# Optimization experiments

Hardware: AMD Instinct MI355X
Metric: run time of the kernel (lower is better)

## Reference

```python
import jax, jax.numpy as jnp
import numpy as np

N_NODES = 50000
N_REL = 8
N_EDGES = 400000  # per relation
D_IN = 256
D_OUT = 256


def setup_inputs() -> dict:
    key = jax.random.key(0)
    k1, k2, k3, k4, k5 = jax.random.split(key, 5)
    gain = np.sqrt(2.0)  # relu gain used by xavier init in the module
    x = jax.random.normal(k1, (N_NODES, D_IN), dtype=jnp.float32)
    weight = jax.random.normal(k2, (N_REL, D_IN, D_OUT), dtype=jnp.float32) * (gain / np.sqrt(D_IN + D_OUT))
    h_bias = jnp.zeros((D_OUT,), dtype=jnp.float32)
    loop_weight = jax.random.normal(k3, (D_IN, D_OUT), dtype=jnp.float32) * (gain / np.sqrt(D_IN + D_OUT))
    src_idx = jax.random.randint(k4, (N_REL, N_EDGES), 0, N_NODES, dtype=jnp.int32)
    dst_idx = jax.random.randint(k5, (N_REL, N_EDGES), 0, N_NODES, dtype=jnp.int32)
    return {"x": x, "weight": weight, "h_bias": h_bias, "loop_weight": loop_weight,
            "src_idx": src_idx, "dst_idx": dst_idx}


def reference(x, weight, h_bias, loop_weight, src_idx, dst_idx):
    # x: [N, D_in]; weight: [R, D_in, D_out]; src/dst_idx: [R, E]
    n = x.shape[0]
    out = jnp.zeros((n, weight.shape[-1]), dtype=x.dtype)
    # Loop over the small fixed set of relations (structurally distinct weights).
    for r in range(weight.shape[0]):
        h = x @ weight[r]                                   # [N, D_out] transform-first (in<=out path of GraphConv)
        msg = h[src_idx[r]]                                 # [E, D_out] gather
        agg = jax.ops.segment_sum(msg, dst_idx[r], num_segments=n)  # [N, D_out] scatter-add
        deg = jax.ops.segment_sum(jnp.ones((dst_idx.shape[1],), dtype=x.dtype),
                                  dst_idx[r], num_segments=n)
        out = out + agg / jnp.clip(deg, 1.0)[:, None]       # norm='right': divide by in-degree (clamped at 1)
    out = out + x @ loop_weight + h_bias                    # self-loop + bias
    return jax.nn.relu(out)                                  # activation; dropout(p=0) is identity
```

## Files before the change

### kernel.cpp

```cpp
#include <hip/hip_runtime.h>
#include <hip/hip_bf16.h>

#define NN 50000
#define NPAD 50048
#define NR 8
#define NE 400000
#define CAP 32
#define CHUNK 2048
#define CPB 196
#define NRANGE 6250
#define XBLK 12500
#define TBLK 144

typedef __attribute__((ext_vector_type(8))) short short8v;
typedef __attribute__((ext_vector_type(4))) float f32x4;
typedef __attribute__((ext_vector_type(2))) unsigned int uint2v;

static __device__ __forceinline__ ushort f2b(float f) {
  union { float f; unsigned u; } v; v.f = f;
  unsigned u = v.u;
  unsigned r = (u + 0x7fffu + ((u >> 16) & 1u)) >> 16;
  return (ushort)r;
}
static __device__ __forceinline__ float b2f(ushort u) {
  union { unsigned u; float f; } v; v.u = ((unsigned)u) << 16;
  return v.f;
}


__global__ __launch_bounds__(256) void k_prep(const float* __restrict__ x,
                                              const float* __restrict__ w,
                                              const float* __restrict__ lw,
                                              ushort* __restrict__ xb,
                                              ushort* __restrict__ wb,
                                              const int* __restrict__ src,
                                              const int* __restrict__ dst,
                                              int* __restrict__ cnt,
                                              ushort* __restrict__ csrp) {
  __shared__ ushort tile[64][66];
  int b = blockIdx.x;
  if (b < XBLK) {
    int i = b * 256 + threadIdx.x;
    float4 v = ((const float4*)x)[i];
    ushort4 o;
    o.x = f2b(v.x); o.y = f2b(v.y); o.z = f2b(v.z); o.w = f2b(v.w);
    ((ushort4*)xb)[i] = o;
    return;
  }
  if (b < XBLK + TBLK) {
    int tb = b - XBLK;
    int s = tb >> 4, t16 = tb & 15;
    int kt = (t16 >> 2) * 64, nt2 = (t16 & 3) * 64;
    const float* srcw = (s < 8) ? (w + (size_t)s * 65536) : lw;
    int t = threadIdx.x;
    #pragma unroll
    for (int i = 0; i < 16; ++i) {
      int flat = i * 256 + t;
      int kk = flat >> 6, nn = flat & 63;
      tile[kk][nn] = f2b(srcw[(size_t)(kt + kk) * 256 + nt2 + nn]);
    }
    __syncthreads();
    #pragma unroll
    for (int i = 0; i < 16; ++i) {
      int flat = i * 256 + t;
      int nn2 = flat >> 6, kk2 = flat & 63;
      wb[(size_t)s * 65536 + (size_t)(nt2 + nn2) * 256 + kt + kk2] = tile[kk2][nn2];
    }
    return;
  }
  int xcd = b & 7;
  int rc = (b - XBLK - TBLK) >> 3;
  int r = rc / CPB;
  int c = rc - r * CPB;
  int nlo = xcd * NRANGE, nhi = nlo + NRANGE;
  const int* dr = dst + (size_t)r * NE;
  const int* sr = src + (size_t)r * NE;
  int e0 = c * CHUNK + threadIdx.x * 4;
  #pragma unroll
  for (int u = 0; u < CHUNK / 1024; ++u) {
    int e = e0 + u * 1024;
    if (e + 3 < NE) {
      int4 d4 = *(const int4*)(dr + e);
      int4 s4 = *(const int4*)(sr + e);
      #pragma unroll
      for (int k = 0; k < 4; ++k) {
        int d = (k == 0) ? d4.x : (k == 1) ? d4.y : (k == 2) ? d4.z : d4.w;
        int s = (k == 0) ? s4.x : (k == 1) ? s4.y : (k == 2) ? s4.z : s4.w;
        if (d >= nlo && d < nhi) {
          int slot = atomicAdd(&cnt[r * NN + d], 1);
          if (slot < CAP)
            csrp[((size_t)r * NN + d) * CAP + slot] = (ushort)s;
        }
      }
    } else {
      for (int k = 0; k < 4; ++k) {
        int e2 = e + k;
        if (e2 < NE) {
          int d = dr[e2];
          if (d >= nlo && d < nhi) {
            int slot = atomicAdd(&cnt[r * NN + d], 1);
            if (slot < CAP)
              csrp[((size_t)r * NN + d) * CAP + slot] = (ushort)sr[e2];
          }
        }
      }
    }
  }
}


__global__ __launch_bounds__(256) void k_agg(const ushort* __restrict__ xb,
                                             const ushort* __restrict__ csrp,
                                             const int* __restrict__ cnt,
                                             ushort* __restrict__ xa,
                                             long strideR, int r0) {
  int wid = threadIdx.x >> 6, lane = threadIdx.x & 63;
  int n = blockIdx.x * 4 + wid;
  int r = r0 + blockIdx.y;
  if (n >= NN) return;
  int dg = cnt[r * NN + n];
  int m = min(dg, CAP);
  const ushort* lst = csrp + ((size_t)r * NN + n) * CAP;
  float a0 = 0.f, a1 = 0.f, a2 = 0.f, a3 = 0.f;
  int j = 0;
  for (; j + 3 < m; j += 4) {
    int s0 = lst[j], s1 = lst[j + 1], s2 = lst[j + 2], s3 = lst[j + 3];
    ushort4 v0 = *(const ushort4*)(xb + (size_t)s0 * 256 + lane * 4);
    ushort4 v1 = *(const ushort4*)(xb + (size_t)s1 * 256 + lane * 4);
    ushort4 v2 = *(const ushort4*)(xb + (size_t)s2 * 256 + lane * 4);
    ushort4 v3 = *(const ushort4*)(xb + (size_t)s3 * 256 + lane * 4);
    a0 += (b2f(v0.x) + b2f(v1.x)) + (b2f(v2.x) + b2f(v3.x));
    a1 += (b2f(v0.y) + b2f(v1.y)) + (b2f(v2.y) + b2f(v3.y));
    a2 += (b2f(v0.z) + b2f(v1.z)) + (b2f(v2.z) + b2f(v3.z));
    a3 += (b2f(v0.w) + b2f(v1.w)) + (b2f(v2.w) + b2f(v3.w));
  }
  for (; j < m; ++j) {
    ushort4 v0 = *(const ushort4*)(xb + (size_t)lst[j] * 256 + lane * 4);
    a0 += b2f(v0.x); a1 += b2f(v0.y); a2 += b2f(v0.z); a3 += b2f(v0.w);
  }
  float inv = 1.f / (float)max(dg, 1);
  unsigned w0 = ((unsigned)f2b(a0 * inv)) | (((unsigned)f2b(a1 * inv)) << 16);
  unsigned w1 = ((unsigned)f2b(a2 * inv)) | (((unsigned)f2b(a3 * inv)) << 16);
  uint2v o; o[0] = w0; o[1] = w1;
  __builtin_nontemporal_store(o, (uint2v*)(xa + (size_t)(r - r0) * strideR +
                                           (size_t)n * 256 + lane * 4));
}


#define BK 64

__global__ __launch_bounds__(512, 4) void k_gemm(
    const ushort* __restrict__ xa, long strideR, int nseg,
    const ushort* __restrict__ xb8, const ushort* __restrict__ wb, int wseg0,
    const float* __restrict__ bias, float* __restrict__ out, int first, int final_) {
  __shared__ ushort As[2][128 * BK];
  __shared__ ushort Bs[256 * BK];
  int t = threadIdx.x;
  int lane = t & 63, wid = t >> 6;
  int wm = wid >> 2, wn = wid & 3;
  int i0 = blockIdx.x * 128;
  const int NT = nseg * 4;

  f32x4 acc[4][4];
  #pragma unroll
  for (int a = 0; a < 4; ++a)
    #pragma unroll
    for (int b = 0; b < 4; ++b) acc[a][b] = (f32x4){0.f, 0.f, 0.f, 0.f};

#define STAGE_A(stp, buf) do {                                                  \
    int s_ = (stp) >> 2; int kt_ = ((stp) & 3) * 64;                            \
    const ushort* A_ = (wseg0 + s_ < 8) ? (xa + (size_t)s_ * strideR) : xb8;    \
    _Pragma("unroll")                                                           \
    for (int it = 0; it < 2; ++it) {                                            \
      int c = it * 512 + t; int row = c >> 3, sg = c & 7;                       \
      int sgg = sg ^ (row & 7);                                                 \
      const ushort* ga = A_ + (size_t)(i0 + row) * 256 + kt_ + sgg * 8;         \
      __builtin_amdgcn_global_load_lds(                                         \
          (const __attribute__((address_space(1))) unsigned int*)ga,            \
          (__attribute__((address_space(3))) unsigned int*)(As[buf] + c * 8),   \
          16, 0, 0);                                                            \
    } } while (0)

#define STAGE_B(stp) do {                                                       \
    int s_ = (stp) >> 2; int kt_ = ((stp) & 3) * 64;                            \
    const ushort* W_ = wb + (size_t)(wseg0 + s_) * 65536;                       \
    _Pragma("unroll")                                                           \
    for (int it = 0; it < 4; ++it) {                                            \
      int c = it * 512 + t; int row = c >> 3, sg = c & 7;                       \
      int sgg = sg ^ (row & 7);                                                 \
      const ushort* gb = W_ + (size_t)row * 256 + kt_ + sgg * 8;                \
      __builtin_amdgcn_global_load_lds(                                         \
          (const __attribute__((address_space(1))) unsigned int*)gb,            \
          (__attribute__((address_space(3))) unsigned int*)(Bs + c * 8),        \
          16, 0, 0);                                                            \
    } } while (0)

  STAGE_A(0, 0);
  int cur = 0;
  #pragma unroll 1
  for (int st = 0; st < NT; ++st) {
    __builtin_amdgcn_s_barrier();
    STAGE_B(st);
    if (st + 1 < NT) {
      STAGE_A(st + 1, cur ^ 1);
      asm volatile("s_waitcnt vmcnt(2)" ::: "memory");
    } else {
      asm volatile("s_waitcnt vmcnt(0)" ::: "memory");
    }
    __builtin_amdgcn_sched_barrier(0);
    __builtin_amdgcn_s_barrier();
    __builtin_amdgcn_sched_barrier(0);
    const ushort* Ac = As[cur];
    #pragma unroll
    for (int kk = 0; kk < 2; ++kk) {
      int ko = kk * 32 + (lane >> 4) * 8;
      int kb = ko * 2;
      short8v a_frag[4], b_frag[4];
      #pragma unroll
      for (int mi = 0; mi < 4; ++mi) {
        int row = wm * 64 + mi * 16 + (lane & 15);
        int ba = row * 128 + (kb ^ ((row & 7) << 4));
        a_frag[mi] = *(const short8v*)((const char*)Ac + ba);
      }
      #pragma unroll
      for (int ni = 0; ni < 4; ++ni) {
        int row = wn * 64 + ni * 16 + (lane & 15);
        int ba = row * 128 + (kb ^ ((row & 7) << 4));
        b_frag[ni] = *(const short8v*)((const char*)Bs + ba);
      }
      #pragma unroll
      for (int mi = 0; mi < 4; ++mi)
        #pragma unroll
        for (int ni = 0; ni < 4; ++ni)
          acc[mi][ni] = __builtin_amdgcn_mfma_f32_16x16x32_bf16(
              a_frag[mi], b_frag[ni], acc[mi][ni], 0, 0, 0);
    }
    cur ^= 1;
  }
#undef STAGE_A
#undef STAGE_B

  #pragma unroll
  for (int mi = 0; mi < 4; ++mi) {
    int rbase = i0 + wm * 64 + mi * 16 + ((lane >> 4) << 2);
    #pragma unroll
    for (int ni = 0; ni < 4; ++ni) {
      int col = wn * 64 + ni * 16 + (lane & 15);
      float bv = final_ ? bias[col] : 0.f;
      #pragma unroll
      for (int rg = 0; rg < 4; ++rg) {
        int gm = rbase + rg;
        if (gm < NN) {
          size_t o = (size_t)gm * 256 + col;
          float v = acc[mi][ni][rg];
          if (!first) v += out[o];
          if (final_) v = fmaxf(v + bv, 0.f);
          out[o] = v;
        }
      }
    }
  }
}


extern "C" void kernel_launch(void* const* d_in, const int* in_sizes, int n_in,
                              void* d_out, int out_size, void* d_ws, size_t ws_size,
                              hipStream_t stream) {
  const float* x = (const float*)d_in[0];
  const float* w = (const float*)d_in[1];
  const float* bias = (const float*)d_in[2];
  const float* lw = (const float*)d_in[3];
  const int* src = (const int*)d_in[4];
  const int* dst = (const int*)d_in[5];
  float* out = (float*)d_out;

  char* ws = (char*)d_ws;
  size_t off = 0;
  auto carve = [&](size_t bytes) {
    size_t o = off;
    off = (off + bytes + 255) & ~(size_t)255;
    return o;
  };
  int* cnt = (int*)(ws + carve((size_t)NR * NN * 4));
  ushort* csrp = (ushort*)(ws + carve((size_t)NR * NN * CAP * 2));
  ushort* wb = (ushort*)(ws + carve((size_t)9 * 65536 * 2));
  ushort* xb = (ushort*)(ws + carve((size_t)NPAD * 256 * 2));
  size_t base_bytes = off;
  ushort* xa = (ushort*)(ws + off);
  const size_t segb = (size_t)NPAD * 256 * 2;
  long strideR = (long)NPAD * 256;

  (void)hipMemsetAsync(cnt, 0, (size_t)NR * NN * 4, stream);
  k_prep<<<XBLK + TBLK + 8 * CPB * NR, 256, 0, stream>>>(x, w, lw, xb, wb,
                                                         src, dst, cnt, csrp);

  dim3 gemm_grid(NPAD / 128);
  if (ws_size >= base_bytes + 8 * segb) {
    k_agg<<<dim3((NN + 3) / 4, 8), 256, 0, stream>>>(xb, csrp, cnt, xa, strideR, 0);
    k_gemm<<<gemm_grid, 512, 0, stream>>>(xa, strideR, 9, xb, wb, 0, bias, out, 1, 1);
  } else if (ws_size >= base_bytes + 4 * segb) {
    k_agg<<<dim3((NN + 3) / 4, 4), 256, 0, stream>>>(xb, csrp, cnt, xa, strideR, 0);
    k_gemm<<<gemm_grid, 512, 0, stream>>>(xa, strideR, 4, xb, wb, 0, bias, out, 1, 0);
    k_agg<<<dim3((NN + 3) / 4, 4), 256, 0, stream>>>(xb, csrp, cnt, xa, strideR, 4);
    k_gemm<<<gemm_grid, 512, 0, stream>>>(xa, strideR, 5, xb, wb, 4, bias, out, 0, 1);
  } else {
    for (int r = 0; r < 8; ++r) {
      k_agg<<<dim3((NN + 3) / 4, 1), 256, 0, stream>>>(xb, csrp, cnt, xa, strideR, r);
      k_gemm<<<gemm_grid, 512, 0, stream>>>(xa, strideR, 1, xb, wb, r, bias, out,
                                            (r == 0) ? 1 : 0, 0);
    }
    k_gemm<<<gemm_grid, 512, 0, stream>>>(xa, strideR, 1, xb, wb, 8, bias, out, 0, 1);
  }
  (void)in_sizes; (void)n_in; (void)out_size;
}
```

Baseline: 453.6 us.

## Use column-chunked bf16 layout so gather aggregation stays cache-resident per chunk

Stores bf16 x and the aggregated features as 8 column chunks of 32 features ([8][NPAD][32]) instead of row-major. The aggregation kernel processes one chunk per grid z-slice, using 8 threads per destination node, so each pass gathers from a much smaller working set that can stay in cache. The GEMM A-tile loads are re-addressed for the chunked layout. The cost is smaller, less contiguous gather segments and 8x more aggregation blocks that each re-read CSR lists and counts.

```diff
diff --git a/kernel.cpp b/kernel.cpp
--- a/kernel.cpp
+++ b/kernel.cpp
@@ -28,10 +28,11 @@
 }
 
 
+
 __global__ __launch_bounds__(256) void k_prep(const float* __restrict__ x,
                                               const float* __restrict__ w,
                                               const float* __restrict__ lw,
-                                              ushort* __restrict__ xb,
+                                              ushort* __restrict__ xbc,
                                               ushort* __restrict__ wb,
                                               const int* __restrict__ src,
                                               const int* __restrict__ dst,
@@ -41,10 +42,11 @@
   int b = blockIdx.x;
   if (b < XBLK) {
     int i = b * 256 + threadIdx.x;
+    int n = i >> 6, q = i & 63;
     float4 v = ((const float4*)x)[i];
     ushort4 o;
     o.x = f2b(v.x); o.y = f2b(v.y); o.z = f2b(v.z); o.w = f2b(v.w);
-    ((ushort4*)xb)[i] = o;
+    *(ushort4*)(xbc + ((size_t)(q >> 3) * NPAD + n) * 32 + (q & 7) * 4) = o;
     return;
   }
   if (b < XBLK + TBLK) {
@@ -109,33 +111,36 @@
 }
 
 
-__global__ __launch_bounds__(256) void k_agg(const ushort* __restrict__ xb,
-                                             const ushort* __restrict__ csrp,
-                                             const int* __restrict__ cnt,
-                                             ushort* __restrict__ xa,
-                                             long strideR, int r0) {
-  int wid = threadIdx.x >> 6, lane = threadIdx.x & 63;
-  int n = blockIdx.x * 4 + wid;
+__global__ __launch_bounds__(256) void k_aggc(const ushort* __restrict__ xbc,
+                                              const ushort* __restrict__ csrp,
+                                              const int* __restrict__ cnt,
+                                              ushort* __restrict__ xa,
+                                              long strideR, int r0) {
+  int t = threadIdx.x;
+  int gl = t & 7;
+  int n = blockIdx.x * 32 + (t >> 3);
   int r = r0 + blockIdx.y;
+  int c = blockIdx.z;
   if (n >= NN) return;
   int dg = cnt[r * NN + n];
   int m = min(dg, CAP);
   const ushort* lst = csrp + ((size_t)r * NN + n) * CAP;
+  const ushort* xc = xbc + (size_t)c * NPAD * 32;
   float a0 = 0.f, a1 = 0.f, a2 = 0.f, a3 = 0.f;
   int j = 0;
   for (; j + 3 < m; j += 4) {
     int s0 = lst[j], s1 = lst[j + 1], s2 = lst[j + 2], s3 = lst[j + 3];
-    ushort4 v0 = *(const ushort4*)(xb + (size_t)s0 * 256 + lane * 4);
-    ushort4 v1 = *(const ushort4*)(xb + (size_t)s1 * 256 + lane * 4);
-    ushort4 v2 = *(const ushort4*)(xb + (size_t)s2 * 256 + lane * 4);
-    ushort4 v3 = *(const ushort4*)(xb + (size_t)s3 * 256 + lane * 4);
+    ushort4 v0 = *(const ushort4*)(xc + (size_t)s0 * 32 + gl * 4);
+    ushort4 v1 = *(const ushort4*)(xc + (size_t)s1 * 32 + gl * 4);
+    ushort4 v2 = *(const ushort4*)(xc + (size_t)s2 * 32 + gl * 4);
+    ushort4 v3 = *(const ushort4*)(xc + (size_t)s3 * 32 + gl * 4);
     a0 += (b2f(v0.x) + b2f(v1.x)) + (b2f(v2.x) + b2f(v3.x));
     a1 += (b2f(v0.y) + b2f(v1.y)) + (b2f(v2.y) + b2f(v3.y));
     a2 += (b2f(v0.z) + b2f(v1.z)) + (b2f(v2.z) + b2f(v3.z));
     a3 += (b2f(v0.w) + b2f(v1.w)) + (b2f(v2.w) + b2f(v3.w));
   }
   for (; j < m; ++j) {
-    ushort4 v0 = *(const ushort4*)(xb + (size_t)lst[j] * 256 + lane * 4);
+    ushort4 v0 = *(const ushort4*)(xc + (size_t)lst[j] * 32 + gl * 4);
     a0 += b2f(v0.x); a1 += b2f(v0.y); a2 += b2f(v0.z); a3 += b2f(v0.w);
   }
   float inv = 1.f / (float)max(dg, 1);
@@ -143,7 +148,7 @@
   unsigned w1 = ((unsigned)f2b(a2 * inv)) | (((unsigned)f2b(a3 * inv)) << 16);
   uint2v o; o[0] = w0; o[1] = w1;
   __builtin_nontemporal_store(o, (uint2v*)(xa + (size_t)(r - r0) * strideR +
-                                           (size_t)n * 256 + lane * 4));
+                                           ((size_t)c * NPAD + n) * 32 + gl * 4));
 }
 
 
@@ -174,7 +179,9 @@
     for (int it = 0; it < 2; ++it) {                                            \
       int c = it * 512 + t; int row = c >> 3, sg = c & 7;                       \
       int sgg = sg ^ (row & 7);                                                 \
-      const ushort* ga = A_ + (size_t)(i0 + row) * 256 + kt_ + sgg * 8;         \
+      int col = kt_ + sgg * 8;                                                  \
+      const ushort* ga = A_ + ((size_t)(col >> 5) * NPAD + (i0 + row)) * 32     \
+                            + (col & 31);                                       \
       __builtin_amdgcn_global_load_lds(                                         \
           (const __attribute__((address_space(1))) unsigned int*)ga,            \
           (__attribute__((address_space(3))) unsigned int*)(As[buf] + c * 8),   \
@@ -284,32 +291,33 @@
   int* cnt = (int*)(ws + carve((size_t)NR * NN * 4));
   ushort* csrp = (ushort*)(ws + carve((size_t)NR * NN * CAP * 2));
   ushort* wb = (ushort*)(ws + carve((size_t)9 * 65536 * 2));
-  ushort* xb = (ushort*)(ws + carve((size_t)NPAD * 256 * 2));
+  ushort* xbc = (ushort*)(ws + carve((size_t)NPAD * 256 * 2));
   size_t base_bytes = off;
   ushort* xa = (ushort*)(ws + off);
   const size_t segb = (size_t)NPAD * 256 * 2;
   long strideR = (long)NPAD * 256;
 
   (void)hipMemsetAsync(cnt, 0, (size_t)NR * NN * 4, stream);
-  k_prep<<<XBLK + TBLK + 8 * CPB * NR, 256, 0, stream>>>(x, w, lw, xb, wb,
+  k_prep<<<XBLK + TBLK + 8 * CPB * NR, 256, 0, stream>>>(x, w, lw, xbc, wb,
                                                          src, dst, cnt, csrp);
 
   dim3 gemm_grid(NPAD / 128);
+  dim3 agg_grid((NN + 31) / 32, 8, 8);
   if (ws_size >= base_bytes + 8 * segb) {
-    k_agg<<<dim3((NN + 3) / 4, 8), 256, 0, stream>>>(xb, csrp, cnt, xa, strideR, 0);
-    k_gemm<<<gemm_grid, 512, 0, stream>>>(xa, strideR, 9, xb, wb, 0, bias, out, 1, 1);
+    k_aggc<<<agg_grid, 256, 0, stream>>>(xbc, csrp, cnt, xa, strideR, 0);
+    k_gemm<<<gemm_grid, 512, 0, stream>>>(xa, strideR, 9, xbc, wb, 0, bias, out, 1, 1);
   } else if (ws_size >= base_bytes + 4 * segb) {
-    k_agg<<<dim3((NN + 3) / 4, 4), 256, 0, stream>>>(xb, csrp, cnt, xa, strideR, 0);
-    k_gemm<<<gemm_grid, 512, 0, stream>>>(xa, strideR, 4, xb, wb, 0, bias, out, 1, 0);
-    k_agg<<<dim3((NN + 3) / 4, 4), 256, 0, stream>>>(xb, csrp, cnt, xa, strideR, 4);
-    k_gemm<<<gemm_grid, 512, 0, stream>>>(xa, strideR, 5, xb, wb, 4, bias, out, 0, 1);
+    k_aggc<<<dim3((NN + 31) / 32, 4, 8), 256, 0, stream>>>(xbc, csrp, cnt, xa, strideR, 0);
+    k_gemm<<<gemm_grid, 512, 0, stream>>>(xa, strideR, 4, xbc, wb, 0, bias, out, 1, 0);
+    k_aggc<<<dim3((NN + 31) / 32, 4, 8), 256, 0, stream>>>(xbc, csrp, cnt, xa, strideR, 4);
+    k_gemm<<<gemm_grid, 512, 0, stream>>>(xa, strideR, 5, xbc, wb, 4, bias, out, 0, 1);
   } else {
     for (int r = 0; r < 8; ++r) {
-      k_agg<<<dim3((NN + 3) / 4, 1), 256, 0, stream>>>(xb, csrp, cnt, xa, strideR, r);
-      k_gemm<<<gemm_grid, 512, 0, stream>>>(xa, strideR, 1, xb, wb, r, bias, out,
+      k_aggc<<<dim3((NN + 31) / 32, 1, 8), 256, 0, stream>>>(xbc, csrp, cnt, xa, strideR, r);
+      k_gemm<<<gemm_grid, 512, 0, stream>>>(xa, strideR, 1, xbc, wb, r, bias, out,
                                             (r == 0) ? 1 : 0, 0);
     }
-    k_gemm<<<gemm_grid, 512, 0, stream>>>(xa, strideR, 1, xb, wb, 8, bias, out, 0, 1);
+    k_gemm<<<gemm_grid, 512, 0, stream>>>(xa, strideR, 1, xbc, wb, 8, bias, out, 0, 1);
   }
   (void)in_sizes; (void)n_in; (void)out_size;
 }
```

Measured after the change: 492.8 us. 1.09x slower.
